# Kernel optimization log

Hardware: AMD Instinct MI355X
Metric: run time of the kernel (lower is better)

The kernel has to match this reference:

```python
import jax, jax.numpy as jnp
import numpy as np

LOSS_WEIGHT = 1.0
RADIUS = 1
DILATION = 2

def _mind_shift_indices():
    # six-neighbourhood offsets in a 3x3x3 kernel (as in torch code)
    six = np.array([[0, 1, 1], [1, 1, 0], [1, 0, 1], [1, 1, 2], [2, 1, 1], [1, 2, 1]])
    dist = ((six[:, None, :] - six[None, :, :]) ** 2).sum(-1)
    x, y = np.meshgrid(np.arange(6), np.arange(6), indexing='ij')
    mask = ((x > y) & (dist == 2)).reshape(-1)
    idx1 = np.repeat(six, 6, axis=0)[mask]
    idx2 = np.tile(six, (6, 1))[mask]
    return idx1, idx2

_IDX1, _IDX2 = _mind_shift_indices()

def _shifted(padded, idx, d, D, H, W):
    # one-hot dilated conv == static slice of replication-padded volume
    outs = [padded[:, :, a * d:a * d + D, b * d:b * d + H, c * d:c * d + W]
            for (a, b, c) in idx]
    return jnp.concatenate(outs, axis=1)  # (N, 12, D, H, W)

def mind_ssc(img, radius=RADIUS, dilation=DILATION):
    N, C, D, H, W = img.shape
    p = dilation
    padded = jnp.pad(img, ((0, 0), (0, 0), (p, p), (p, p), (p, p)), mode='edge')
    diff2 = (_shifted(padded, _IDX1, dilation, D, H, W)
             - _shifted(padded, _IDX2, dilation, D, H, W)) ** 2
    r = radius
    k = 2 * r + 1
    diff2p = jnp.pad(diff2, ((0, 0), (0, 0), (r, r), (r, r), (r, r)), mode='edge')
    ssd = jax.lax.reduce_window(diff2p, 0.0, jax.lax.add,
                                (1, 1, k, k, k), (1, 1, 1, 1, 1), 'VALID') / (k ** 3)
    mind = ssd - jnp.min(ssd, axis=1, keepdims=True)
    mind_var = jnp.mean(mind, axis=1, keepdims=True)
    m = jax.lax.stop_gradient(jnp.mean(mind_var))  # torch uses .item() -> detached
    mind_var = jnp.clip(mind_var, m * 0.001, m * 1000.0)
    return jnp.exp(-mind / mind_var)

def setup_inputs() -> dict:
    key = jax.random.key(0)
    k1, k2 = jax.random.split(key)
    shape = (2, 1, 128, 128, 128)
    predict = jax.random.normal(k1, shape, dtype=jnp.float32)
    target = jax.random.normal(k2, shape, dtype=jnp.float32)
    return {"predict": predict, "target": target}

def reference(predict, target):
    loss = jnp.mean((mind_ssc(predict) - mind_ssc(target)) ** 2)
    return loss * LOSS_WEIGHT
```

## Files before the change

### kernel.cpp

```cpp
#include <hip/hip_runtime.h>


#define DIM 128
#define HW (128 * 128)
#define DHW (128 * 128 * 128)
#define NVOX (2 * DHW)
#define LOSS_COUNT (2.0 * 12.0 * DHW)
#define TOTAL_BLOCKS 1024u

#define TS   16
#define SY   18
#define NSP  (SY * TS)
#define CHZ  16
#define PSTR 7

typedef float f4 __attribute__((ext_vector_type(4)));
typedef float f2 __attribute__((ext_vector_type(2)));

__device__ __forceinline__ int clampi(int v) {
    v = v < 0 ? 0 : v;
    return v > 127 ? 127 : v;
}

__device__ __forceinline__ unsigned fkey(float f) {
    unsigned u = __float_as_uint(f);
    return (u & 0x80000000u) ? ~u : (u | 0x80000000u);
}
__device__ __forceinline__ float fdec(unsigned k) {
    unsigned u = (k & 0x80000000u) ? (k ^ 0x80000000u) : ~k;
    return __uint_as_float(u);
}

__device__ __forceinline__ void block_reduce_atomic(float v, double* dst) {
#pragma unroll
    for (int off = 32; off > 0; off >>= 1)
        v += __shfl_down(v, off, 64);
    __shared__ float red[4];
    int lane = threadIdx.x & 63;
    int wid  = threadIdx.x >> 6;
    if (lane == 0) red[wid] = v;
    __syncthreads();
    if (threadIdx.x == 0) {
        double t = (double)red[0] + (double)red[1] + (double)red[2] + (double)red[3];
        atomicAdd(dst, t);
    }
    __syncthreads();
}

__device__ __forceinline__ void block_minmax_atomic(float mnp, float mxp,
                                                    float mnt, float mxt,
                                                    unsigned* keys) {
#pragma unroll
    for (int off = 32; off > 0; off >>= 1) {
        mnp = fminf(mnp, __shfl_down(mnp, off, 64));
        mxp = fmaxf(mxp, __shfl_down(mxp, off, 64));
        mnt = fminf(mnt, __shfl_down(mnt, off, 64));
        mxt = fmaxf(mxt, __shfl_down(mxt, off, 64));
    }
    __shared__ float r[4][4];
    int lane = threadIdx.x & 63, wid = threadIdx.x >> 6;
    if (lane == 0) { r[wid][0] = mnp; r[wid][1] = mxp; r[wid][2] = mnt; r[wid][3] = mxt; }
    __syncthreads();
    if (threadIdx.x == 0) {
        float a = fminf(fminf(r[0][0], r[1][0]), fminf(r[2][0], r[3][0]));
        float b = fmaxf(fmaxf(r[0][1], r[1][1]), fmaxf(r[2][1], r[3][1]));
        float c = fminf(fminf(r[0][2], r[1][2]), fminf(r[2][2], r[3][2]));
        float d = fmaxf(fmaxf(r[0][3], r[1][3]), fmaxf(r[2][3], r[3][3]));
        atomicMax(&keys[0], ~fkey(a));
        atomicMax(&keys[1], fkey(b));
        atomicMax(&keys[2], ~fkey(c));
        atomicMax(&keys[3], fkey(d));
    }
    __syncthreads();
}

struct SPos {
    int y0, ym, yp;
    int cx[3], cm[3], cp[3];
    int woff;
};

__device__ __forceinline__ SPos make_spos(int p, int y0t, int x0t, int stride) {
    SPos q;
    int py = p >> 4, px = p & 15;
    int gy = clampi(y0t - 1 + py);
    int gx = x0t + px;
    q.y0 = gy * DIM; q.ym = clampi(gy - 2) * DIM; q.yp = clampi(gy + 2) * DIM;
#pragma unroll
    for (int wx = 0; wx < 3; ++wx) {
        int c = clampi(gx + wx - 1);
        q.cx[wx] = c;
        q.cm[wx] = clampi(c - 2);
        q.cp[wx] = clampi(c + 2);
    }
    q.woff = p * stride;
    return q;
}


__device__ __forceinline__ void stage_pair(const float* __restrict__ ip,
                                           const float* __restrict__ tp,
                                           int zm, int zc, int zp,
                                           const SPos& q, f4* __restrict__ X) {
    f2 acc[12];
#pragma unroll
    for (int c = 0; c < 12; ++c) acc[c] = (f2)0.0f;
#pragma unroll
    for (int wx = 0; wx < 3; ++wx) {
        int o0 = zm + q.y0 + q.cx[wx];
        int o1 = zc + q.y0 + q.cm[wx];
        int o2 = zc + q.ym + q.cx[wx];
        int o3 = zc + q.y0 + q.cp[wx];
        int o4 = zp + q.y0 + q.cx[wx];
        int o5 = zc + q.yp + q.cx[wx];
        f2 s0 = {ip[o0], tp[o0]};
        f2 s1 = {ip[o1], tp[o1]};
        f2 s2 = {ip[o2], tp[o2]};
        f2 s3 = {ip[o3], tp[o3]};
        f2 s4 = {ip[o4], tp[o4]};
        f2 s5 = {ip[o5], tp[o5]};
        f2 d;
        d = s1 - s0; acc[0]  += d * d;
        d = s2 - s0; acc[1]  += d * d;
        d = s2 - s1; acc[2]  += d * d;
        d = s3 - s0; acc[3]  += d * d;
        d = s3 - s2; acc[4]  += d * d;
        d = s4 - s1; acc[5]  += d * d;
        d = s4 - s2; acc[6]  += d * d;
        d = s4 - s3; acc[7]  += d * d;
        d = s5 - s0; acc[8]  += d * d;
        d = s5 - s1; acc[9]  += d * d;
        d = s5 - s3; acc[10] += d * d;
        d = s5 - s4; acc[11] += d * d;
    }
#pragma unroll
    for (int k = 0; k < 6; ++k) {
        f4 w;
        w.x = acc[2 * k].x;     w.y = acc[2 * k].y;
        w.z = acc[2 * k + 1].x; w.w = acc[2 * k + 1].y;
        X[q.woff + k] = w;
    }
}

__device__ __forceinline__ void box3y_pair(const f4* __restrict__ X,
                                           int ty, int tx, f4 q[6]) {
    int b0 = ((ty + 0) * TS + tx) * PSTR;
    int b1 = ((ty + 1) * TS + tx) * PSTR;
    int b2 = ((ty + 2) * TS + tx) * PSTR;
#pragma unroll
    for (int k = 0; k < 6; ++k)
        q[k] = X[b0 + k] + X[b1 + k] + X[b2 + k];
}

__global__ __launch_bounds__(256, 4) void fused_kernel(const float* __restrict__ pred,
                                                       const float* __restrict__ targ,
                                                       double* __restrict__ acc,
                                                       unsigned* __restrict__ keys) {
    __shared__ f4 X[NSP * PSTR];
    const int t = threadIdx.x;
    const int tile = blockIdx.x & 63, n = blockIdx.x >> 6;
    const int x0t = (tile & 7) * TS, y0t = (tile >> 3) * TS;
    const int z0 = blockIdx.y * CHZ;
    const float* ip = pred + (size_t)n * DHW;
    const float* tp = targ + (size_t)n * DHW;

    SPos pa = make_spos(t, y0t, x0t, PSTR);
    const bool hasB = (t + 256) < NSP;
    SPos pb = make_spos(hasB ? (t + 256) : 0, y0t, x0t, PSTR);

    const int ty = t >> 4, tx = t & 15;

    f4 A[6], B[6];
#pragma unroll
    for (int k = 0; k < 6; ++k) { A[k] = (f4)0.0f; B[k] = (f4)0.0f; }

    float vsump = 0.0f, vsumt = 0.0f, lsum = 0.0f;
    float locmnp = 1e30f, locmxp = -1e30f, locmnt = 1e30f, locmxt = -1e30f;

    for (int tz = z0 - 1; tz <= z0 + CHZ; ++tz) {
        int zq = clampi(tz);
        int zc = zq * HW, zm = clampi(zq - 2) * HW, zp = clampi(zq + 2) * HW;
        stage_pair(ip, tp, zm, zc, zp, pa, X);
        if (hasB) stage_pair(ip, tp, zm, zc, zp, pb, X);
        __syncthreads();

        f4 q[6];
        box3y_pair(X, ty, tx, q);
        __syncthreads();

        int ze = tz - 1;
        if (ze >= z0) {
            f4 v[6];
#pragma unroll
            for (int k = 0; k < 6; ++k) v[k] = A[k] + q[k];

            float mnp = v[0][0], mnt = v[0][1];
            float smp = 0.0f, smt = 0.0f;
#pragma unroll
            for (int c = 0; c < 12; ++c) {
                float pv = v[c >> 1][(c & 1) * 2];
                float tv = v[c >> 1][(c & 1) * 2 + 1];
                mnp = fminf(mnp, pv); smp += pv;
                mnt = fminf(mnt, tv); smt += tv;
            }
            float varp = smp * (1.0f / 12.0f) - mnp;
            float vart = smt * (1.0f / 12.0f) - mnt;
            vsump += varp; vsumt += vart;
            locmnp = fminf(locmnp, varp); locmxp = fmaxf(locmxp, varp);
            locmnt = fminf(locmnt, vart); locmxt = fmaxf(locmxt, vart);

            float invp = -1.0f / varp;
            float invt = -1.0f / vart;
            float la = 0.0f;
#pragma unroll
            for (int c = 0; c < 12; ++c) {
                float pv = v[c >> 1][(c & 1) * 2];
                float tv = v[c >> 1][(c & 1) * 2 + 1];
                float ep = __expf((pv - mnp) * invp);
                float et = __expf((tv - mnt) * invt);
                float dd = ep - et;
                la += dd * dd;
            }
            lsum += la;
        }
#pragma unroll
        for (int k = 0; k < 6; ++k) { A[k] = B[k] + q[k]; B[k] = q[k]; }
    }

    block_reduce_atomic(vsump, &acc[0]);
    block_reduce_atomic(vsumt, &acc[1]);
    block_reduce_atomic(lsum,  &acc[2]);
    block_minmax_atomic(locmnp, locmxp, locmnt, locmxt, keys);
}


__device__ __forceinline__ void stage_xsum(const float* __restrict__ im,
                                           int zm, int zc, int zp,
                                           const SPos& q, f4* __restrict__ P) {
    f4 a = (f4)0.0f, b = (f4)0.0f, c = (f4)0.0f;
#pragma unroll
    for (int wx = 0; wx < 3; ++wx) {
        float s0 = im[zm + q.y0 + q.cx[wx]];
        float s1 = im[zc + q.y0 + q.cm[wx]];
        float s2 = im[zc + q.ym + q.cx[wx]];
        float s3 = im[zc + q.y0 + q.cp[wx]];
        float s4 = im[zp + q.y0 + q.cx[wx]];
        float s5 = im[zc + q.yp + q.cx[wx]];
        float d;
        d = s1 - s0; a.x += d * d;
        d = s2 - s0; a.y += d * d;
        d = s2 - s1; a.z += d * d;
        d = s3 - s0; a.w += d * d;
        d = s3 - s2; b.x += d * d;
        d = s4 - s1; b.y += d * d;
        d = s4 - s2; b.z += d * d;
        d = s4 - s3; b.w += d * d;
        d = s5 - s0; c.x += d * d;
        d = s5 - s1; c.y += d * d;
        d = s5 - s3; c.z += d * d;
        d = s5 - s4; c.w += d * d;
    }
    P[q.woff + 0] = a;
    P[q.woff + 1] = b;
    P[q.woff + 2] = c;
}

__device__ __forceinline__ void box3y(const f4* __restrict__ P,
                                      int ty, int tx, f4 q[3]) {
    int base = (ty * TS + tx) * 3;
#pragma unroll
    for (int k = 0; k < 3; ++k)
        q[k] = P[base + k] + P[base + TS * 3 + k] + P[base + 2 * TS * 3 + k];
}

__device__ __forceinline__ float min12(const f4 v[3]) {
    float mn = v[0][0];
#pragma unroll
    for (int i = 0; i < 4; ++i)
        mn = fminf(mn, fminf(v[0][i], fminf(v[1][i], v[2][i])));
    return mn;
}
__device__ __forceinline__ float sum12(const f4 v[3]) {
    float sm = 0.0f;
#pragma unroll
    for (int i = 0; i < 4; ++i)
        sm += v[0][i] + v[1][i] + v[2][i];
    return sm;
}

__global__ __launch_bounds__(256, 4) void combo_kernel(const float* __restrict__ pred,
                                                       const float* __restrict__ targ,
                                                       double* __restrict__ acc,
                                                       unsigned* __restrict__ keys,
                                                       float* __restrict__ out) {
    const float m_p = (float)(acc[0] * (1.0 / (double)NVOX));
    const float m_t = (float)(acc[1] * (1.0 / (double)NVOX));
    const float mnp = fdec(~keys[0]), mxp = fdec(keys[1]);
    const float mnt = fdec(~keys[2]), mxt = fdec(keys[3]);
    const bool clean = (mnp >= m_p * 0.001f) && (mxp <= m_p * 1000.0f) &&
                       (mnt >= m_t * 0.001f) && (mxt <= m_t * 1000.0f);
    if (clean) {
        if (blockIdx.x == 0 && blockIdx.y == 0 && threadIdx.x == 0)
            out[0] = (float)(acc[2] * (1.0 / LOSS_COUNT));
        return;
    }

    __shared__ f4 Xp[NSP * 3];
    __shared__ f4 Xt[NSP * 3];
    const int t = threadIdx.x;
    const int tile = blockIdx.x & 63, n = blockIdx.x >> 6;
    const int x0t = (tile & 7) * TS, y0t = (tile >> 3) * TS;
    const int z0 = blockIdx.y * CHZ;
    const float* ip = pred + (size_t)n * DHW;
    const float* tp = targ + (size_t)n * DHW;

    SPos pa = make_spos(t, y0t, x0t, 3);
    const bool hasB = (t + 256) < NSP;
    SPos pb = make_spos(hasB ? (t + 256) : 0, y0t, x0t, 3);

    const int ty = t >> 4, tx = t & 15;

    f4 Ap[3], Bp[3], At[3], Bt[3];
#pragma unroll
    for (int q = 0; q < 3; ++q) {
        Ap[q] = (f4)0.0f; Bp[q] = (f4)0.0f;
        At[q] = (f4)0.0f; Bt[q] = (f4)0.0f;
    }
    float lsum = 0.0f;

    for (int tz = z0 - 1; tz <= z0 + CHZ; ++tz) {
        int zq = clampi(tz);
        int zc = zq * HW, zm = clampi(zq - 2) * HW, zp = clampi(zq + 2) * HW;
        stage_xsum(ip, zm, zc, zp, pa, Xp);
        stage_xsum(tp, zm, zc, zp, pa, Xt);
        if (hasB) {
            stage_xsum(ip, zm, zc, zp, pb, Xp);
            stage_xsum(tp, zm, zc, zp, pb, Xt);
        }
        __syncthreads();

        f4 qp[3], qt[3];
        box3y(Xp, ty, tx, qp);
        box3y(Xt, ty, tx, qt);
        __syncthreads();

        int ze = tz - 1;
        if (ze >= z0) {
            f4 vp[3], vt[3];
#pragma unroll
            for (int q = 0; q < 3; ++q) {
                vp[q] = Ap[q] + qp[q];
                vt[q] = At[q] + qt[q];
            }
            float mnpv = min12(vp), smp = sum12(vp);
            float mntv = min12(vt), smt = sum12(vt);
            float varp = smp * (1.0f / 12.0f) - mnpv;
            varp = fminf(fmaxf(varp, m_p * 0.001f), m_p * 1000.0f);
            float invp = -1.0f / varp;
            float vart = smt * (1.0f / 12.0f) - mntv;
            vart = fminf(fmaxf(vart, m_t * 0.001f), m_t * 1000.0f);
            float invt = -1.0f / vart;

            float a = 0.0f;
#pragma unroll
            for (int q = 0; q < 3; ++q)
#pragma unroll
                for (int i = 0; i < 4; ++i) {
                    float ep = __expf((vp[q][i] - mnpv) * invp);
                    float et = __expf((vt[q][i] - mntv) * invt);
                    float dd = ep - et;
                    a += dd * dd;
                }
            lsum += a;
        }
#pragma unroll
        for (int q = 0; q < 3; ++q) {
            Ap[q] = Bp[q] + qp[q]; Bp[q] = qp[q];
            At[q] = Bt[q] + qt[q]; Bt[q] = qt[q];
        }
    }

    block_reduce_atomic(lsum, &acc[3]);

    __threadfence();
    if (threadIdx.x == 0) {
        unsigned old = atomicAdd(&keys[6], 1u);
        if (old == TOTAL_BLOCKS - 1u) {
            __threadfence();
            double v = atomicAdd(&acc[3], 0.0);
            out[0] = (float)(v * (1.0 / LOSS_COUNT));
        }
    }
}

extern "C" void kernel_launch(void* const* d_in, const int* in_sizes, int n_in,
                              void* d_out, int out_size, void* d_ws, size_t ws_size,
                              hipStream_t stream) {
    const float* pred = (const float*)d_in[0];
    const float* targ = (const float*)d_in[1];
    float* out = (float*)d_out;
    double* acc = (double*)d_ws;
    unsigned* keys = (unsigned*)((char*)d_ws + 64);

    dim3 block(256);
    dim3 grid(128, 8);

    hipMemsetAsync(d_ws, 0, 256, stream);
    fused_kernel<<<grid, block, 0, stream>>>(pred, targ, acc, keys);
    combo_kernel<<<grid, block, 0, stream>>>(pred, targ, acc, keys, out);
}
```

Before: 169.1 us.

## Stage current z-plane tile with halo in double-buffered LDS for in-plane neighbours

The fused kernel now loads a 22x24 halo tile of the current z-plane for both images into a double-buffered shared-memory ring, prefetching the next plane while the current one is used. The four in-plane neighbour samples (x±2, y±2) are read from LDS instead of global memory, and edge-clamp cases that the tile cannot represent fall back to global loads. This cuts redundant global/L2 traffic from overlapping stencils. In exchange it adds shared memory (lower occupancy risk), extra index bookkeeping and branchy fallback paths.

```diff
diff --git a/kernel.cpp b/kernel.cpp
--- a/kernel.cpp
+++ b/kernel.cpp
@@ -13,6 +13,12 @@
 #define NSP  (SY * TS)
 #define CHZ  16
 #define PSTR 7
+
+#define RSTR  24
+#define RROWS 22
+#define RIMG  (RROWS * RSTR)
+#define RSLOT (2 * RIMG)
+#define RITEMS (2 * RIMG)
 
 typedef float f4 __attribute__((ext_vector_type(4)));
 typedef float f2 __attribute__((ext_vector_type(2)));
@@ -74,64 +80,82 @@
     __syncthreads();
 }
 
-struct SPos {
+
+struct SPosF {
     int y0, ym, yp;
-    int cx[3], cm[3], cp[3];
+    int cx0, cx1, cx2;
+    int cm2, cp0;
     int woff;
+    int l_y0;
+    bool exc_ym, exc_yp, exc_s1, exc_s3;
 };
 
-__device__ __forceinline__ SPos make_spos(int p, int y0t, int x0t, int stride) {
-    SPos q;
-    int py = p >> 4, px = p & 15;
+__device__ __forceinline__ SPosF make_sposf(int p, int y0t, int x0t) {
+    SPosF q;
+    int py = p >> 4, tx = p & 15;
     int gy = clampi(y0t - 1 + py);
-    int gx = x0t + px;
+    int gx = x0t + tx;
     q.y0 = gy * DIM; q.ym = clampi(gy - 2) * DIM; q.yp = clampi(gy + 2) * DIM;
-#pragma unroll
-    for (int wx = 0; wx < 3; ++wx) {
-        int c = clampi(gx + wx - 1);
-        q.cx[wx] = c;
-        q.cm[wx] = clampi(c - 2);
-        q.cp[wx] = clampi(c + 2);
-    }
-    q.woff = p * stride;
+    q.cx0 = clampi(gx - 1);
+    q.cx1 = gx;
+    q.cx2 = clampi(gx + 1);
+    q.cm2 = clampi(q.cx2 - 2);
+    q.cp0 = clampi(q.cx0 + 2);
+    q.woff = p * PSTR;
+    q.l_y0 = (py + 2) * RSTR + tx;
+    q.exc_ym = (y0t == 112) && (py == 17);
+    q.exc_yp = (y0t == 0)   && (py == 0);
+    q.exc_s1 = (x0t == 112) && (tx == 15);
+    q.exc_s3 = (x0t == 0)   && (tx == 0);
     return q;
 }
 
+
+__device__ __forceinline__ void acc12(f2 acc[12], f2 s0, f2 s1, f2 s2,
+                                      f2 s3, f2 s4, f2 s5) {
+    f2 d;
+    d = s1 - s0; acc[0]  += d * d;
+    d = s2 - s0; acc[1]  += d * d;
+    d = s2 - s1; acc[2]  += d * d;
+    d = s3 - s0; acc[3]  += d * d;
+    d = s3 - s2; acc[4]  += d * d;
+    d = s4 - s1; acc[5]  += d * d;
+    d = s4 - s2; acc[6]  += d * d;
+    d = s4 - s3; acc[7]  += d * d;
+    d = s5 - s0; acc[8]  += d * d;
+    d = s5 - s1; acc[9]  += d * d;
+    d = s5 - s3; acc[10] += d * d;
+    d = s5 - s4; acc[11] += d * d;
+}
 
 __device__ __forceinline__ void stage_pair(const float* __restrict__ ip,
                                            const float* __restrict__ tp,
                                            int zm, int zc, int zp,
-                                           const SPos& q, f4* __restrict__ X) {
+                                           const float* Rc,
+                                           const SPosF& q, f4* __restrict__ X) {
     f2 acc[12];
 #pragma unroll
     for (int c = 0; c < 12; ++c) acc[c] = (f2)0.0f;
+
+    const int ly0 = q.l_y0;
+    const int lym = q.l_y0 - 2 * RSTR;
+    const int lyp = q.l_y0 + 2 * RSTR;
 #pragma unroll
     for (int wx = 0; wx < 3; ++wx) {
-        int o0 = zm + q.y0 + q.cx[wx];
-        int o1 = zc + q.y0 + q.cm[wx];
-        int o2 = zc + q.ym + q.cx[wx];
-        int o3 = zc + q.y0 + q.cp[wx];
-        int o4 = zp + q.y0 + q.cx[wx];
-        int o5 = zc + q.yp + q.cx[wx];
+        const int cxw = (wx == 0) ? q.cx0 : (wx == 1 ? q.cx1 : q.cx2);
+        int o0 = zm + q.y0 + cxw;
+        int o4 = zp + q.y0 + cxw;
         f2 s0 = {ip[o0], tp[o0]};
-        f2 s1 = {ip[o1], tp[o1]};
-        f2 s2 = {ip[o2], tp[o2]};
-        f2 s3 = {ip[o3], tp[o3]};
         f2 s4 = {ip[o4], tp[o4]};
-        f2 s5 = {ip[o5], tp[o5]};
-        f2 d;
-        d = s1 - s0; acc[0]  += d * d;
-        d = s2 - s0; acc[1]  += d * d;
-        d = s2 - s1; acc[2]  += d * d;
-        d = s3 - s0; acc[3]  += d * d;
-        d = s3 - s2; acc[4]  += d * d;
-        d = s4 - s1; acc[5]  += d * d;
-        d = s4 - s2; acc[6]  += d * d;
-        d = s4 - s3; acc[7]  += d * d;
-        d = s5 - s0; acc[8]  += d * d;
-        d = s5 - s1; acc[9]  += d * d;
-        d = s5 - s3; acc[10] += d * d;
-        d = s5 - s4; acc[11] += d * d;
+        f2 s1 = {Rc[ly0 + wx],         Rc[RIMG + ly0 + wx]};
+        f2 s3 = {Rc[ly0 + 4 + wx],     Rc[RIMG + ly0 + 4 + wx]};
+        f2 s2 = {Rc[lym + 2 + wx],     Rc[RIMG + lym + 2 + wx]};
+        f2 s5 = {Rc[lyp + 2 + wx],     Rc[RIMG + lyp + 2 + wx]};
+        if (wx == 2 && q.exc_s1) { int o = zc + q.y0 + q.cm2; s1 = {ip[o], tp[o]}; }
+        if (wx == 0 && q.exc_s3) { int o = zc + q.y0 + q.cp0; s3 = {ip[o], tp[o]}; }
+        if (q.exc_ym)            { int o = zc + q.ym + cxw;   s2 = {ip[o], tp[o]}; }
+        if (q.exc_yp)            { int o = zc + q.yp + cxw;   s5 = {ip[o], tp[o]}; }
+        acc12(acc, s0, s1, s2, s3, s4, s5);
     }
 #pragma unroll
     for (int k = 0; k < 6; ++k) {
@@ -157,6 +181,7 @@
                                                        double* __restrict__ acc,
                                                        unsigned* __restrict__ keys) {
     __shared__ f4 X[NSP * PSTR];
+    __shared__ float R[2 * RSLOT];
     const int t = threadIdx.x;
     const int tile = blockIdx.x & 63, n = blockIdx.x >> 6;
     const int x0t = (tile & 7) * TS, y0t = (tile >> 3) * TS;
@@ -164,9 +189,23 @@
     const float* ip = pred + (size_t)n * DHW;
     const float* tp = targ + (size_t)n * DHW;
 
-    SPos pa = make_spos(t, y0t, x0t, PSTR);
+    SPosF pa = make_sposf(t, y0t, x0t);
     const bool hasB = (t + 256) < NSP;
-    SPos pb = make_spos(hasB ? (t + 256) : 0, y0t, x0t, PSTR);
+    SPosF pb = make_sposf(hasB ? (t + 256) : 0, y0t, x0t);
+
+    int sdst[5], ssrc[5]; bool simg[5];
+#pragma unroll
+    for (int j = 0; j < 5; ++j) {
+        int idx = t + j * 256;
+        if (idx < RITEMS) {
+            int img = idx >= RIMG;
+            int e = idx - img * RIMG;
+            int r = e / RSTR, c = e - r * RSTR;
+            sdst[j] = img * RIMG + e;
+            ssrc[j] = clampi(y0t - 3 + r) * DIM + clampi(x0t - 3 + c);
+            simg[j] = (img != 0);
+        } else sdst[j] = -1;
+    }
 
     const int ty = t >> 4, tx = t & 15;
 
@@ -176,12 +215,32 @@
 
     float vsump = 0.0f, vsumt = 0.0f, lsum = 0.0f;
     float locmnp = 1e30f, locmxp = -1e30f, locmnt = 1e30f, locmxt = -1e30f;
+
+    {
+        int pzHW = clampi(z0 - 1) * HW;
+        float* Rs = R + ((unsigned)(z0 - 1) & 1u) * RSLOT;
+#pragma unroll
+        for (int j = 0; j < 5; ++j)
+            if (sdst[j] >= 0) Rs[sdst[j]] = (simg[j] ? tp : ip)[pzHW + ssrc[j]];
+    }
+    __syncthreads();
 
     for (int tz = z0 - 1; tz <= z0 + CHZ; ++tz) {
         int zq = clampi(tz);
         int zc = zq * HW, zm = clampi(zq - 2) * HW, zp = clampi(zq + 2) * HW;
-        stage_pair(ip, tp, zm, zc, zp, pa, X);
-        if (hasB) stage_pair(ip, tp, zm, zc, zp, pb, X);
+        int slot = tz & 1;
+
+        if (tz < z0 + CHZ) {
+            int pzHW = clampi(tz + 1) * HW;
+            float* Rs = R + (slot ^ 1) * RSLOT;
+#pragma unroll
+            for (int j = 0; j < 5; ++j)
+                if (sdst[j] >= 0) Rs[sdst[j]] = (simg[j] ? tp : ip)[pzHW + ssrc[j]];
+        }
+
+        const float* Rc = R + slot * RSLOT;
+        stage_pair(ip, tp, zm, zc, zp, Rc, pa, X);
+        if (hasB) stage_pair(ip, tp, zm, zc, zp, Rc, pb, X);
         __syncthreads();
 
         f4 q[6];
@@ -233,6 +292,29 @@
     block_minmax_atomic(locmnp, locmxp, locmnt, locmxt, keys);
 }
 
+
+struct SPos {
+    int y0, ym, yp;
+    int cx[3], cm[3], cp[3];
+    int woff;
+};
+
+__device__ __forceinline__ SPos make_spos(int p, int y0t, int x0t, int stride) {
+    SPos q;
+    int py = p >> 4, px = p & 15;
+    int gy = clampi(y0t - 1 + py);
+    int gx = x0t + px;
+    q.y0 = gy * DIM; q.ym = clampi(gy - 2) * DIM; q.yp = clampi(gy + 2) * DIM;
+#pragma unroll
+    for (int wx = 0; wx < 3; ++wx) {
+        int c = clampi(gx + wx - 1);
+        q.cx[wx] = c;
+        q.cm[wx] = clampi(c - 2);
+        q.cp[wx] = clampi(c + 2);
+    }
+    q.woff = p * stride;
+    return q;
+}
 
 __device__ __forceinline__ void stage_xsum(const float* __restrict__ im,
                                            int zm, int zc, int zp,
```

Result: slower. 222.8 us (+31.7%).
